# Performance work log

Measured on AMD Instinct MI355X. Metric: run time of the kernel, lower is better.

The kernel has to match this reference:

```python
import jax, jax.numpy as jnp
import numpy as np

N = 2048   # nodes
E = 8      # edge types (num_edge)
C = 8      # channels (num_channels)


def setup_inputs() -> dict:
    key = jax.random.key(0)
    k0, k1, k2, k3, k4 = jax.random.split(key, 5)
    # adjacency stack [1, N, N, E]; non-negative like adjacency weights
    A = jax.random.uniform(k0, (1, N, N, E), dtype=jnp.float32)
    # GTConv weights [out_channels, in_channels, 1, 1]
    w1_0 = jax.random.normal(k1, (C, E, 1, 1), dtype=jnp.float32) * 0.1
    w2_0 = jax.random.normal(k2, (C, E, 1, 1), dtype=jnp.float32) * 0.1
    w_1 = jax.random.normal(k3, (C, E, 1, 1), dtype=jnp.float32) * 0.1
    w_2 = jax.random.normal(k4, (C, E, 1, 1), dtype=jnp.float32) * 0.1
    return {"A": A, "w1_0": w1_0, "w2_0": w2_0, "w_1": w_1, "w_2": w_2}


def _gtconv(Ap, w):
    # Ap: [1, E, N, N]; w: [C, E, 1, 1] -> softmax over edge-type dim, mix, sum
    sw = jax.nn.softmax(w, axis=1)           # [C, E, 1, 1]
    return jnp.sum(Ap * sw, axis=1)          # [C, N, N]


def _normalize(H):
    # Per channel: zero diagonal, then scale column j by 1/sum_i H[i,j]
    # (equivalent to torch code's transpose -> row degree norm -> transpose)
    n = H.shape[-1]
    Hm = H * (1.0 - jnp.eye(n, dtype=H.dtype))[None]   # [C, N, N] diag zeroed
    deg = jnp.sum(Hm, axis=1)                           # [C, N] column sums
    deg_safe = jnp.where(deg == 0, jnp.ones_like(deg), deg)
    deg_inv = jnp.where(deg == 0, jnp.zeros_like(deg), 1.0 / deg_safe)
    return Hm * deg_inv[:, None, :]


def reference(A, w1_0, w2_0, w_1, w_2):
    Ap = jnp.transpose(A, (0, 3, 1, 2))      # [1, E, N, N]
    a = _gtconv(Ap, w1_0)                    # [C, N, N]
    b = _gtconv(Ap, w2_0)                    # [C, N, N]
    H = jnp.matmul(a, b)                     # batched meta-path product
    for w in (w_1, w_2):
        H = _normalize(H)
        H = jnp.matmul(H, _gtconv(Ap, w))
    Hm = jnp.mean(H, axis=0)                 # [N, N]
    return (Hm + Hm.T) * 0.5
```

## Files before the change

kernel.cpp:

```cpp
#include <hip/hip_runtime.h>
#include <hip/hip_bf16.h>

using short8 = __attribute__((ext_vector_type(8))) short;
using f32x4  = __attribute__((ext_vector_type(4))) float;

#define NN 2048
#define NC 8
static const size_t PLANE = (size_t)NN * NN;

__device__ __forceinline__ void gload16(const void* g, void* l) {
  __builtin_amdgcn_global_load_lds((const __attribute__((address_space(1))) unsigned int*)g,
                                   (__attribute__((address_space(3))) unsigned int*)l, 16, 0, 0);
}

__global__ __launch_bounds__(256) void softmax_w_k(const float* __restrict__ w0, const float* __restrict__ w1,
                                                   const float* __restrict__ w2, const float* __restrict__ w3,
                                                   float* __restrict__ sw) {
  int t = threadIdx.x;
  const float* srcs[4] = {w0, w1, w2, w3};
  float v = srcs[t >> 6][t & 63];
  float m = v;
  #pragma unroll
  for (int d = 1; d < 8; d <<= 1) m = fmaxf(m, __shfl_xor(m, d, 8));
  float ex = __expf(v - m);
  float s = ex;
  #pragma unroll
  for (int d = 1; d < 8; d <<= 1) s += __shfl_xor(s, d, 8);
  sw[t] = ex / s;
}

template<int W4>
__global__ __launch_bounds__(512) void gtconv_fused(const float* __restrict__ A, const float* __restrict__ sw,
                                                    short* __restrict__ a, short* __restrict__ bT,
                                                    short* __restrict__ c1T, short* __restrict__ c2T) {
  __shared__ float tile[16384];
  __shared__ float swl[256];
  const int t = threadIdx.x;
  const int i0 = blockIdx.y * 32, j0 = blockIdx.x * 64;
  if (t < 256) swl[t] = sw[t];

  const float* Abase = A + ((size_t)i0 * NN + j0) * 8;
  #pragma unroll
  for (int q = 0; q < 8; q++) {
    const int d = q * 512 + t;
    const int s = (d & ~15) | ((d ^ (d >> 4)) & 15);
    const int row = s >> 7, fc = s & 127;
    gload16(Abase + (size_t)row * (NN * 8) + fc * 4, &tile[(q * 512 + (t & ~63)) * 4]);
  }
  asm volatile("s_waitcnt vmcnt(0)" ::: "memory");
  __syncthreads();

  {
    const int ch = t & 1, jg = (t >> 1) & 7, ii = t >> 4;
    const int sxx = (ii * 8 + jg) & 15;
    const int fb = ii * 128 + jg * 16;
    float acc[4][8];
    #pragma unroll
    for (int cc = 0; cc < 4; cc++)
      #pragma unroll
      for (int p = 0; p < 8; p++) acc[cc][p] = 0.f;
    #pragma unroll
    for (int p = 0; p < 8; p++) {
      const int k0 = p * 2;
      const float4 v0 = *reinterpret_cast<const float4*>(&tile[((fb & ~15) | (k0 ^ sxx)) * 4]);
      const float4 v1 = *reinterpret_cast<const float4*>(&tile[((fb & ~15) | ((k0 + 1) ^ sxx)) * 4]);
      const float e[8] = {v0.x, v0.y, v0.z, v0.w, v1.x, v1.y, v1.z, v1.w};
      #pragma unroll
      for (int cc = 0; cc < 4; cc++) {
        const int c = ch * 4 + cc;
        #pragma unroll
        for (int k = 0; k < 8; k++) acc[cc][p] += e[k] * swl[c * 8 + k];
      }
    }
    #pragma unroll
    for (int cc = 0; cc < 4; cc++) {
      const int c = ch * 4 + cc;
      short8 o;
      #pragma unroll
      for (int p = 0; p < 8; p++) {
        __hip_bfloat16 hb = __float2bfloat16(acc[cc][p]);
        o[p] = *reinterpret_cast<short*>(&hb);
      }
      *reinterpret_cast<short8*>(a + (size_t)c * PLANE + (size_t)(i0 + ii) * NN + j0 + jg * 8) = o;
    }
  }

  {
    const int ch = t & 1, ig = (t >> 1) & 3, jj = t >> 3;
    const int NT_OUT = W4 ? 3 : 2;
    short* outs[3] = {bT, c1T, c2T};
    #pragma unroll
    for (int T = 0; T < NT_OUT; T++) {
      short* outp = outs[T];
      const float* swt = &swl[(T + 1) * 64];
      float acc[4][8];
      #pragma unroll
      for (int cc = 0; cc < 4; cc++)
        #pragma unroll
        for (int p = 0; p < 8; p++) acc[cc][p] = 0.f;
      #pragma unroll
      for (int p = 0; p < 8; p++) {
        const int irow = ig * 8 + p;
        const int fb = irow * 128 + jj * 2;
        const int sxx = (irow * 8 + (jj >> 3)) & 15;
        const int k0 = fb & 15;
        const float4 v0 = *reinterpret_cast<const float4*>(&tile[((fb & ~15) | (k0 ^ sxx)) * 4]);
        const float4 v1 = *reinterpret_cast<const float4*>(&tile[((fb & ~15) | ((k0 + 1) ^ sxx)) * 4]);
        const float e[8] = {v0.x, v0.y, v0.z, v0.w, v1.x, v1.y, v1.z, v1.w};
        #pragma unroll
        for (int cc = 0; cc < 4; cc++) {
          const int c = ch * 4 + cc;
          #pragma unroll
          for (int k = 0; k < 8; k++) acc[cc][p] += e[k] * swt[c * 8 + k];
        }
      }
      #pragma unroll
      for (int cc = 0; cc < 4; cc++) {
        const int c = ch * 4 + cc;
        short8 o;
        #pragma unroll
        for (int p = 0; p < 8; p++) {
          __hip_bfloat16 hb = __float2bfloat16(acc[cc][p]);
          o[p] = *reinterpret_cast<short*>(&hb);
        }
        *reinterpret_cast<short8*>(outp + (size_t)c * PLANE + (size_t)(j0 + jj) * NN + i0 + ig * 8) = o;
      }
    }
  }
}

__global__ __launch_bounds__(256) void gtconv_one(const float* __restrict__ A, const float* __restrict__ sw,
                                                  __hip_bfloat16* __restrict__ oT) {
  __shared__ float Als[32][33][9];
  __shared__ float swl[8][8];
  int t = threadIdx.x;
  if (t < 64) swl[t >> 3][t & 7] = sw[t];
  int i0 = blockIdx.y * 32, j0 = blockIdx.x * 32;
  #pragma unroll
  for (int q = 0; q < 8; q++) {
    int fi = t + q * 256;
    int e4 = fi & 1, jj = (fi >> 1) & 31, ii = fi >> 6;
    const float4 v = *reinterpret_cast<const float4*>(A + (((size_t)(i0 + ii) * NN + (j0 + jj)) << 3) + e4 * 4);
    float* dst = &Als[ii][jj][e4 * 4];
    dst[0] = v.x; dst[1] = v.y; dst[2] = v.z; dst[3] = v.w;
  }
  __syncthreads();
  #pragma unroll
  for (int q = 0; q < 4; q++) {
    int pos = t + q * 256;
    int r = pos >> 5, s = pos & 31;
    float e[8];
    #pragma unroll
    for (int k = 0; k < 8; k++) e[k] = Als[s][r][k];
    size_t base = (size_t)(j0 + r) * NN + (i0 + s);
    #pragma unroll
    for (int c = 0; c < 8; c++) {
      float v1 = 0.f;
      #pragma unroll
      for (int k = 0; k < 8; k++) v1 += e[k] * swl[c][k];
      oT[(size_t)c * PLANE + base] = __float2bfloat16(v1);
    }
  }
}

#define GBM 256
#define GBK 64
template<int CPB, int PARTIALS>
__global__ __launch_bounds__(512, 2) void gemm8(const short* __restrict__ Ag0, const short* __restrict__ Bg0,
                                                float* __restrict__ C, float* __restrict__ degp) {
  __shared__ short lds[65536];
  __shared__ float colred[2][256];
  const int t = threadIdx.x;
  const int lane = t & 63, w = t >> 6;
  const int wr = w >> 2, wc = w & 3;
  const int m0 = blockIdx.y * GBM, n0 = blockIdx.x * GBM;
  const short* Abase = Ag0 + (size_t)blockIdx.z * CPB * PLANE;
  const short* Bbase = Bg0 + (size_t)blockIdx.z * CPB * PLANE;
  const int NT = CPB * 32;

  const int lrow = t >> 3;
  const int lk8  = t & 7;
  const int fr = lane & 15, fk = (lane >> 4) * 8;

  f32x4 acc[8][4] = {};

  auto STAGE = [&](int tt, int p) {
    const int k0 = (tt & 31) * GBK;
    const short* Ag = Abase + (size_t)(tt >> 5) * PLANE;
    const short* Bg = Bbase + (size_t)(tt >> 5) * PLANE;
    #pragma unroll
    for (int q = 0; q < 4; q++) {
      const int row = q * 64 + lrow;
      const int ksrc = ((lk8 ^ (row & 7)) * 8);
      short* la = &lds[p * 32768 +         q * 4096 + w * 512];
      short* lb = &lds[p * 32768 + 16384 + q * 4096 + w * 512];
      gload16(Ag + (size_t)(m0 + row) * NN + k0 + ksrc, la);
      gload16(Bg + (size_t)(n0 + row) * NN + k0 + ksrc, lb);
    }
  };

  STAGE(0, 0);
  STAGE(1, 1);
  asm volatile("s_waitcnt vmcnt(8)" ::: "memory");
  __builtin_amdgcn_sched_barrier(0);
  __builtin_amdgcn_s_barrier();
  __builtin_amdgcn_sched_barrier(0);

  short8 aq[8][2], bq[4][2];

#define RD_AH(H, PC)                                                                       \
  { _Pragma("unroll") for (int m = 0; m < 4; m++) {                                        \
      const int row = wr * 128 + ((H) * 4 + m) * 16 + fr;                                  \
      const int sw8 = (row & 7) * 8;                                                       \
      _Pragma("unroll") for (int kx = 0; kx < 2; kx++)                                     \
        aq[(H) * 4 + m][kx] = *reinterpret_cast<const short8*>(&(PC)[row * 64 + ((kx * 32 + fk) ^ sw8)]); } }

#define RD_BH(H, PC)                                                                       \
  { _Pragma("unroll") for (int n = 0; n < 2; n++) {                                        \
      const int row = wc * 64 + ((H) * 2 + n) * 16 + fr;                                   \
      const int sw8 = (row & 7) * 8;                                                       \
      _Pragma("unroll") for (int kx = 0; kx < 2; kx++)                                     \
        bq[(H) * 2 + n][kx] = *reinterpret_cast<const short8*>(&(PC)[16384 + row * 64 + ((kx * 32 + fk) ^ sw8)]); } }

#define QCL(MH, NH)                                                                        \
  { __builtin_amdgcn_s_setprio(1);                                                         \
    _Pragma("unroll") for (int kx = 0; kx < 2; kx++)                                       \
      _Pragma("unroll") for (int m = 0; m < 4; m++)                                        \
        _Pragma("unroll") for (int n = 0; n < 2; n++)                                      \
          acc[(MH) * 4 + m][(NH) * 2 + n] = __builtin_amdgcn_mfma_f32_16x16x32_bf16(       \
              aq[(MH) * 4 + m][kx], bq[(NH) * 2 + n][kx], acc[(MH) * 4 + m][(NH) * 2 + n], 0, 0, 0); \
    __builtin_amdgcn_s_setprio(0); }

  for (int tt = 0; tt < NT; ++tt) {
    const int p = tt & 1;
    const short* pc = &lds[p * 32768];

    RD_AH(0, pc); RD_BH(0, pc);
    __builtin_amdgcn_sched_barrier(0);
    QCL(0, 0);
    __builtin_amdgcn_sched_barrier(0);
    RD_AH(1, pc); RD_BH(1, pc);
    __builtin_amdgcn_sched_barrier(0);
    QCL(1, 0);
    __builtin_amdgcn_sched_barrier(0);
    QCL(0, 1);
    __builtin_amdgcn_sched_barrier(0);
    QCL(1, 1);
    __builtin_amdgcn_sched_barrier(0);

    __builtin_amdgcn_s_barrier();
    __builtin_amdgcn_sched_barrier(0);
    if (tt + 2 < NT) {
      STAGE(tt + 2, p);
      asm volatile("s_waitcnt vmcnt(8)" ::: "memory");
    } else {
      asm volatile("s_waitcnt vmcnt(0)" ::: "memory");
    }
    __builtin_amdgcn_sched_barrier(0);
    __builtin_amdgcn_s_barrier();
    __builtin_amdgcn_sched_barrier(0);
  }
#undef RD_AH
#undef RD_BH
#undef QCL

  float* Cg = C + (size_t)blockIdx.z * PLANE;
  const int orow = (lane >> 4) * 4, ocol = lane & 15;
  #pragma unroll
  for (int m = 0; m < 8; m++)
    #pragma unroll
    for (int n = 0; n < 4; n++) {
      const int gr = m0 + wr * 128 + m * 16 + orow;
      const int gc = n0 + wc * 64 + n * 16 + ocol;
      #pragma unroll
      for (int j = 0; j < 4; j++)
        Cg[(size_t)(gr + j) * NN + gc] = acc[m][n][j];
    }

  if (PARTIALS) {
    #pragma unroll
    for (int n = 0; n < 4; n++) {
      float s = 0.f;
      #pragma unroll
      for (int m = 0; m < 8; m++)
        #pragma unroll
        for (int j = 0; j < 4; j++) s += acc[m][n][j];
      s += __shfl_xor(s, 16);
      s += __shfl_xor(s, 32);
      if (lane < 16) colred[wr][wc * 64 + n * 16 + lane] = s;
    }
    __syncthreads();
    if (t < 256) {
      float s = colred[0][t] + colred[1][t];
      degp[((size_t)blockIdx.z * 8 + blockIdx.y) * NN + n0 + t] = s;
    }
  }
}

__global__ __launch_bounds__(256) void reduce_inv(const float* __restrict__ degp, const float* __restrict__ H,
                                                  float* __restrict__ deginv) {
  int idx = blockIdx.x * 256 + threadIdx.x;
  int c = idx >> 11, j = idx & (NN - 1);
  float s = 0.f;
  #pragma unroll
  for (int tb = 0; tb < 8; tb++) s += degp[((size_t)c * 8 + tb) * NN + j];
  s -= H[(size_t)c * PLANE + (size_t)j * NN + j];
  deginv[idx] = (s == 0.f) ? 0.f : 1.f / s;
}

__global__ __launch_bounds__(256) void normalize_cast(const float* __restrict__ H, const float* __restrict__ deginv,
                                                      short* __restrict__ Hn) {
  size_t idx = (size_t)blockIdx.x * 256 + threadIdx.x;
  size_t e0 = idx * 8;
  int c = (int)(e0 >> 22);
  size_t rem = e0 & (PLANE - 1);
  int i = (int)(rem >> 11), j0 = (int)(rem & (NN - 1));
  const float4 h0 = *reinterpret_cast<const float4*>(H + e0);
  const float4 h1 = *reinterpret_cast<const float4*>(H + e0 + 4);
  const float4 d0 = *reinterpret_cast<const float4*>(deginv + c * NN + j0);
  const float4 d1 = *reinterpret_cast<const float4*>(deginv + c * NN + j0 + 4);
  float v[8] = {h0.x * d0.x, h0.y * d0.y, h0.z * d0.z, h0.w * d0.w,
                h1.x * d1.x, h1.y * d1.y, h1.z * d1.z, h1.w * d1.w};
  int dd = i - j0;
  if (dd >= 0 && dd < 8) v[dd] = 0.f;
  short8 o;
  #pragma unroll
  for (int k = 0; k < 8; k++) {
    __hip_bfloat16 hb = __float2bfloat16(v[k]);
    o[k] = *reinterpret_cast<short*>(&hb);
  }
  *reinterpret_cast<short8*>(Hn + e0) = o;
}

__global__ __launch_bounds__(256) void final_sym4(const float* __restrict__ M, float* __restrict__ out) {
  __shared__ float tl[64][65];
  int t = threadIdx.x;
  int i0 = blockIdx.y * 64, j0 = blockIdx.x * 64;
  int r0 = t >> 6, cl = t & 63;
  float acc[16];
  #pragma unroll
  for (int q = 0; q < 16; q++) acc[q] = 0.f;
  for (int p = 0; p < 4; p++) {
    const float* Mp = M + (size_t)p * PLANE;
    __syncthreads();
    #pragma unroll
    for (int q = 0; q < 16; q++) {
      int rr = r0 + q * 4;
      tl[rr][cl] = Mp[(size_t)(j0 + rr) * NN + i0 + cl];
    }
    __syncthreads();
    #pragma unroll
    for (int q = 0; q < 16; q++) {
      int rr = r0 + q * 4;
      acc[q] += Mp[(size_t)(i0 + rr) * NN + j0 + cl] + tl[cl][rr];
    }
  }
  #pragma unroll
  for (int q = 0; q < 16; q++) {
    int rr = r0 + q * 4;
    out[(size_t)(i0 + rr) * NN + j0 + cl] = acc[q] * (1.0f / 16.0f);
  }
}

extern "C" void kernel_launch(void* const* d_in, const int* in_sizes, int n_in,
                              void* d_out, int out_size, void* d_ws, size_t ws_size,
                              hipStream_t stream) {
  const float* A    = (const float*)d_in[0];
  const float* w1_0 = (const float*)d_in[1];
  const float* w2_0 = (const float*)d_in[2];
  const float* w_1  = (const float*)d_in[3];
  const float* w_2  = (const float*)d_in[4];
  float* out = (float*)d_out;

  char* w = (char*)d_ws;
  float* sw     = (float*)w;
  float* degp   = (float*)(w + (1 << 17));
  float* deginv = (float*)(w + (1 << 17) + (1 << 21));
  const size_t BSZ = (size_t)NC * PLANE * sizeof(short);
  short* B0 = (short*)(w + (4u << 20));
  short* B1 = (short*)((char*)B0 + BSZ);
  short* B2 = (short*)((char*)B1 + BSZ);
  const size_t HSZ = (size_t)NC * PLANE * sizeof(float);
  const size_t need4 = (4u << 20) + 4 * BSZ + HSZ;
  const bool fused4 = ws_size >= need4;
  short* B3 = (short*)((char*)B2 + BSZ);
  float* HH = fused4 ? (float*)((char*)B3 + BSZ) : (float*)((char*)B2 + BSZ);

  dim3 blk(256), blkg(512);
  dim3 gfuse(NN / 64, NN / 32);
  dim3 gconv(64, 64);
  dim3 ggemm(8, 8, 8);
  dim3 ggemm4(8, 8, 4);

  softmax_w_k<<<1, blk, 0, stream>>>(w1_0, w2_0, w_1, w_2, sw);
  if (fused4) {
    gtconv_fused<1><<<gfuse, blkg, 0, stream>>>(A, sw, B0, B1, B2, B3);
  } else {
    gtconv_fused<0><<<gfuse, blkg, 0, stream>>>(A, sw, B0, B1, B2, B3);
  }

  gemm8<1, 1><<<ggemm, blkg, 0, stream>>>(B0, B1, HH, degp);
  reduce_inv<<<64, blk, 0, stream>>>(degp, HH, deginv);
  normalize_cast<<<16384, blk, 0, stream>>>(HH, deginv, B0);
  if (!fused4) {
    gtconv_one<<<gconv, blk, 0, stream>>>(A, sw + 192, (__hip_bfloat16*)B1);
  }

  gemm8<1, 1><<<ggemm, blkg, 0, stream>>>(B0, B2, HH, degp);
  reduce_inv<<<64, blk, 0, stream>>>(degp, HH, deginv);
  normalize_cast<<<16384, blk, 0, stream>>>(HH, deginv, B0);

  short* Bc2 = fused4 ? B3 : B1;
  gemm8<2, 0><<<ggemm4, blkg, 0, stream>>>(B0, Bc2, HH, degp);
  final_sym4<<<dim3(32, 32), blk, 0, stream>>>(HH, out);
}
```

Before: 672.5 us.

## Interleave quarter-tile global-to-LDS loads with MFMA phases in gemm8 main loop

Restructures the bf16 GEMM main loop into a ping-ponged, two-tiles-per-iteration schedule. Each LDS stage is split into four quarter loads, which are issued between the four MFMA sub-phases instead of in one burst after compute. Fragment registers are split so only half the A fragments and a quarter of the B fragments are live at a time, lowering register pressure. In exchange it adds barriers and lgkmcnt waits around every MFMA phase, and the prefetch distance is tighter, which could stall on memory latency.

```diff
diff --git a/kernel.cpp b/kernel.cpp
--- a/kernel.cpp
+++ b/kernel.cpp
@@ -177,6 +177,7 @@
   const short* Abase = Ag0 + (size_t)blockIdx.z * CPB * PLANE;
   const short* Bbase = Bg0 + (size_t)blockIdx.z * CPB * PLANE;
   const int NT = CPB * 32;
+  const int NITER = NT / 2;
 
   const int lrow = t >> 3;
   const int lk8  = t & 7;
@@ -184,85 +185,97 @@
 
   f32x4 acc[8][4] = {};
 
-  auto STAGE = [&](int tt, int p) {
+  auto STAGEH = [&](int tt, int h) {
     const int k0 = (tt & 31) * GBK;
-    const short* Ag = Abase + (size_t)(tt >> 5) * PLANE;
-    const short* Bg = Bbase + (size_t)(tt >> 5) * PLANE;
-    #pragma unroll
-    for (int q = 0; q < 4; q++) {
-      const int row = q * 64 + lrow;
+    const int pl = tt >> 5;
+    const short* G = (h & 2) ? (Bbase + (size_t)pl * PLANE) : (Abase + (size_t)pl * PLANE);
+    const int rb = (h & 2) ? n0 : m0;
+    #pragma unroll
+    for (int q = 0; q < 2; q++) {
+      const int row = (h & 1) * 128 + q * 64 + lrow;
       const int ksrc = ((lk8 ^ (row & 7)) * 8);
-      short* la = &lds[p * 32768 +         q * 4096 + w * 512];
-      short* lb = &lds[p * 32768 + 16384 + q * 4096 + w * 512];
-      gload16(Ag + (size_t)(m0 + row) * NN + k0 + ksrc, la);
-      gload16(Bg + (size_t)(n0 + row) * NN + k0 + ksrc, lb);
+      short* l = &lds[(tt & 1) * 32768 + (h & 2) * 8192 + (h & 1) * 8192 + q * 4096 + w * 512];
+      gload16(G + (size_t)(rb + row) * NN + k0 + ksrc, l);
     }
   };
 
-  STAGE(0, 0);
-  STAGE(1, 1);
-  asm volatile("s_waitcnt vmcnt(8)" ::: "memory");
-  __builtin_amdgcn_sched_barrier(0);
-  __builtin_amdgcn_s_barrier();
-  __builtin_amdgcn_sched_barrier(0);
-
-  short8 aq[8][2], bq[4][2];
-
-#define RD_AH(H, PC)                                                                       \
-  { _Pragma("unroll") for (int m = 0; m < 4; m++) {                                        \
-      const int row = wr * 128 + ((H) * 4 + m) * 16 + fr;                                  \
-      const int sw8 = (row & 7) * 8;                                                       \
-      _Pragma("unroll") for (int kx = 0; kx < 2; kx++)                                     \
-        aq[(H) * 4 + m][kx] = *reinterpret_cast<const short8*>(&(PC)[row * 64 + ((kx * 32 + fk) ^ sw8)]); } }
-
-#define RD_BH(H, PC)                                                                       \
-  { _Pragma("unroll") for (int n = 0; n < 2; n++) {                                        \
-      const int row = wc * 64 + ((H) * 2 + n) * 16 + fr;                                   \
-      const int sw8 = (row & 7) * 8;                                                       \
-      _Pragma("unroll") for (int kx = 0; kx < 2; kx++)                                     \
-        bq[(H) * 2 + n][kx] = *reinterpret_cast<const short8*>(&(PC)[16384 + row * 64 + ((kx * 32 + fk) ^ sw8)]); } }
-
-#define QCL(MH, NH)                                                                        \
-  { __builtin_amdgcn_s_setprio(1);                                                         \
+  short8 af0[4][2], af1[4][2], bq[2][2];
+
+#define RD_AF(AF, MH, PC) { _Pragma("unroll") for (int m = 0; m < 4; m++) {                \
+    const int row = wr * 128 + ((MH) * 4 + m) * 16 + fr;                                   \
+    const int sw8 = (row & 7) * 8;                                                         \
+    _Pragma("unroll") for (int kx = 0; kx < 2; kx++)                                       \
+      AF[m][kx] = *reinterpret_cast<const short8*>(&(PC)[row * 64 + ((kx * 32 + fk) ^ sw8)]); } }
+
+#define RD_BF(NH, PC) { _Pragma("unroll") for (int n = 0; n < 2; n++) {                    \
+    const int row = wc * 64 + ((NH) * 2 + n) * 16 + fr;                                    \
+    const int sw8 = (row & 7) * 8;                                                         \
+    _Pragma("unroll") for (int kx = 0; kx < 2; kx++)                                       \
+      bq[n][kx] = *reinterpret_cast<const short8*>(&(PC)[16384 + row * 64 + ((kx * 32 + fk) ^ sw8)]); } }
+
+#define QMM(AF, MH, NH) { __builtin_amdgcn_s_setprio(1);                                   \
     _Pragma("unroll") for (int kx = 0; kx < 2; kx++)                                       \
       _Pragma("unroll") for (int m = 0; m < 4; m++)                                        \
         _Pragma("unroll") for (int n = 0; n < 2; n++)                                      \
           acc[(MH) * 4 + m][(NH) * 2 + n] = __builtin_amdgcn_mfma_f32_16x16x32_bf16(       \
-              aq[(MH) * 4 + m][kx], bq[(NH) * 2 + n][kx], acc[(MH) * 4 + m][(NH) * 2 + n], 0, 0, 0); \
+              AF[m][kx], bq[n][kx], acc[(MH) * 4 + m][(NH) * 2 + n], 0, 0, 0);             \
     __builtin_amdgcn_s_setprio(0); }
 
-  for (int tt = 0; tt < NT; ++tt) {
-    const int p = tt & 1;
-    const short* pc = &lds[p * 32768];
-
-    RD_AH(0, pc); RD_BH(0, pc);
+#define PH_PRE { __builtin_amdgcn_sched_barrier(0); __builtin_amdgcn_s_barrier();          \
+    asm volatile("s_waitcnt lgkmcnt(0)" ::: "memory"); __builtin_amdgcn_sched_barrier(0); }
+#define PH_POST { __builtin_amdgcn_sched_barrier(0); __builtin_amdgcn_s_barrier();         \
+    __builtin_amdgcn_sched_barrier(0); }
+
+  STAGEH(0, 0); STAGEH(0, 1); STAGEH(0, 2); STAGEH(0, 3);
+  STAGEH(1, 0); STAGEH(1, 1);
+  asm volatile("s_waitcnt vmcnt(4)" ::: "memory");
+  __builtin_amdgcn_sched_barrier(0);
+  __builtin_amdgcn_s_barrier();
+  __builtin_amdgcn_sched_barrier(0);
+
+  const short* c0 = &lds[0];
+  const short* c1 = &lds[32768];
+
+  for (int it = 0; it < NITER; ++it) {
+    const int t1 = it * 2 + 1, f2 = it * 2 + 2, f3 = it * 2 + 3;
+    const bool more = (it + 1 < NITER);
+
+    RD_AF(af0, 0, c0); RD_BF(0, c0);
+    STAGEH(t1, 2);
+    PH_PRE; QMM(af0, 0, 0); PH_POST;
+    RD_AF(af1, 1, c0);
+    STAGEH(t1, 3);
+    PH_PRE; QMM(af1, 1, 0); PH_POST;
+    RD_BF(1, c0);
+    if (more) STAGEH(f2, 0);
+    PH_PRE; QMM(af0, 0, 1); PH_POST;
+    if (more) STAGEH(f2, 1);
+    PH_PRE; QMM(af1, 1, 1);
     __builtin_amdgcn_sched_barrier(0);
-    QCL(0, 0);
+    if (more) { asm volatile("s_waitcnt vmcnt(4)" ::: "memory"); }
+    else      { asm volatile("s_waitcnt vmcnt(0)" ::: "memory"); }
+    PH_POST;
+    RD_AF(af0, 0, c1); RD_BF(0, c1);
+    if (more) STAGEH(f2, 2);
+    PH_PRE; QMM(af0, 0, 0); PH_POST;
+    RD_AF(af1, 1, c1);
+    if (more) STAGEH(f2, 3);
+    PH_PRE; QMM(af1, 1, 0); PH_POST;
+    RD_BF(1, c1);
+    if (more) STAGEH(f3, 0);
+    PH_PRE; QMM(af0, 0, 1); PH_POST;
+    if (more) STAGEH(f3, 1);
+    PH_PRE; QMM(af1, 1, 1);
     __builtin_amdgcn_sched_barrier(0);
-    RD_AH(1, pc); RD_BH(1, pc);
-    __builtin_amdgcn_sched_barrier(0);
-    QCL(1, 0);
-    __builtin_amdgcn_sched_barrier(0);
-    QCL(0, 1);
-    __builtin_amdgcn_sched_barrier(0);
-    QCL(1, 1);
-    __builtin_amdgcn_sched_barrier(0);
-
-    __builtin_amdgcn_s_barrier();
-    __builtin_amdgcn_sched_barrier(0);
-    if (tt + 2 < NT) {
-      STAGE(tt + 2, p);
-      asm volatile("s_waitcnt vmcnt(8)" ::: "memory");
-    } else {
-      asm volatile("s_waitcnt vmcnt(0)" ::: "memory");
-    }
-    __builtin_amdgcn_sched_barrier(0);
-    __builtin_amdgcn_s_barrier();
-    __builtin_amdgcn_sched_barrier(0);
-  }
-#undef RD_AH
-#undef RD_BH
-#undef QCL
+    if (more) { asm volatile("s_waitcnt vmcnt(4)" ::: "memory"); }
+    else      { asm volatile("s_waitcnt vmcnt(0)" ::: "memory"); }
+    PH_POST;
+  }
+#undef RD_AF
+#undef RD_BF
+#undef QMM
+#undef PH_PRE
+#undef PH_POST
 
   float* Cg = C + (size_t)blockIdx.z * PLANE;
   const int orow = (lane >> 4) * 4, ocol = lane & 15;
```

Measured after the change: 854.9 us. 27.1% more time.
